# Optimization experiments

Hardware: AMD Instinct MI355X
Metric: run time of the kernel (lower is better)

Reference implementation:

```python
import jax, jax.numpy as jnp
import numpy as np

N = 32768          # nodes
LEVELS = 4         # num_sign_hops + 1
NUM_FEATURES = 512
HIDDEN = 512
VQ_DIM = 64
CODEBOOK_SIZE = 4096
VQ_WEIGHT = 0.25   # commitment_weight


def setup_inputs() -> dict:
    key = jax.random.key(0)
    ks = jax.random.split(key, 11)
    s = 0.02
    return {
        "x": jax.random.normal(ks[0], (N, LEVELS, NUM_FEATURES), jnp.float32),
        # per-level encoder: Linear(F,512) -> ReLU -> Linear(512,D)
        "enc_w1": jax.random.normal(ks[1], (LEVELS, NUM_FEATURES, HIDDEN), jnp.float32) * s,
        "enc_b1": jnp.zeros((LEVELS, HIDDEN), jnp.float32),
        "enc_w2": jax.random.normal(ks[2], (LEVELS, HIDDEN, VQ_DIM), jnp.float32) * s,
        "enc_b2": jnp.zeros((LEVELS, VQ_DIM), jnp.float32),
        # per-level decoder: Linear(D,512) -> ReLU -> Linear(512,F)
        "dec_w1": jax.random.normal(ks[3], (LEVELS, VQ_DIM, HIDDEN), jnp.float32) * s,
        "dec_b1": jnp.zeros((LEVELS, HIDDEN), jnp.float32),
        "dec_w2": jax.random.normal(ks[4], (LEVELS, HIDDEN, NUM_FEATURES), jnp.float32) * s,
        "dec_b2": jnp.zeros((LEVELS, NUM_FEATURES), jnp.float32),
        # per-level EMA codebooks (constants w.r.t. gradient in the torch module)
        "codebook": jax.random.normal(ks[5], (LEVELS, CODEBOOK_SIZE, VQ_DIM), jnp.float32),
    }


def reference(x, enc_w1, enc_b1, enc_w2, enc_b2,
              dec_w1, dec_b1, dec_w2, dec_b2, codebook):
    # Faithful to Quantizer.forward (eval mode: dropout = identity; EMA codebook
    # update is a training-time side effect, not part of the returned math).
    L = x.shape[1]
    total_mse = jnp.float32(0.0)
    commit_last = jnp.float32(0.0)
    for l in range(L):  # small fixed level count, structurally distinct params
        xl = x[:, l, :]                                   # [N, F]
        h = jax.nn.relu(xl @ enc_w1[l] + enc_b1[l])       # [N, 512]
        z = h @ enc_w2[l] + enc_b2[l]                     # [N, D]
        cb = codebook[l]                                  # [K, D]
        # squared euclidean distances [N, K] (cdist^2 via expansion)
        d = ((z * z).sum(-1, keepdims=True)
             - 2.0 * (z @ cb.T)
             + (cb * cb).sum(-1)[None, :])
        idx = jnp.argmin(d, axis=-1)                      # [N]
        q = cb[idx]                                       # [N, D] codebook lookup
        # commitment loss: mse(stop_grad(quantize), z) * weight
        commit = VQ_WEIGHT * jnp.mean((jax.lax.stop_gradient(q) - z) ** 2)
        # straight-through estimator
        quant = z + jax.lax.stop_gradient(q - z)
        h2 = jax.nn.relu(quant @ dec_w1[l] + dec_b1[l])   # [N, 512]
        x_hat = h2 @ dec_w2[l] + dec_b2[l]                # [N, F]
        total_mse = total_mse + jnp.mean((x_hat - xl) ** 2)
        commit_last = commit  # original returns LAST level's commit_loss / levels
    return (total_mse / L, commit_last / L)
```

## Files before the change

### kernel.cpp

```cpp
#include <hip/hip_runtime.h>

#define NS 32768
#define NLEV 4
#define NF 512
#define HID 512
#define VQD 64
#define CBS 4096

typedef __attribute__((ext_vector_type(8))) short bf16x8;
typedef __attribute__((ext_vector_type(4))) float f32x4;

#define MFMA16(a, b, c) __builtin_amdgcn_mfma_f32_16x16x32_bf16(a, b, c, 0, 0, 0)

__device__ inline unsigned short f2bf(float f) {
    unsigned int u = __float_as_uint(f);
    unsigned int r = (u + 0x7FFFu + ((u >> 16) & 1u)) >> 16;
    return (unsigned short)r;
}
__device__ inline float bf2f(unsigned short s) {
    return __uint_as_float(((unsigned int)s) << 16);
}

__device__ __forceinline__ void gl16(const void* g, void* l) {
    __builtin_amdgcn_global_load_lds(
        (const __attribute__((address_space(1))) unsigned int*)g,
        (__attribute__((address_space(3))) unsigned int*)l, 16, 0, 0);
}


__global__ void transpose_all(const float* __restrict__ ew1, const float* __restrict__ ew2,
                              const float* __restrict__ dw1, const float* __restrict__ dw2,
                              unsigned short* __restrict__ ew1t, unsigned short* __restrict__ ew2t,
                              unsigned short* __restrict__ dw1t, unsigned short* __restrict__ dw2t) {
    long i = (long)blockIdx.x * 256 + threadIdx.x;
    const long s1 = (long)NLEV * NF * HID;
    const long s2 = (long)NLEV * HID * VQD;
    const long s3 = (long)NLEV * VQD * HID;
    const long s4 = (long)NLEV * HID * NF;
    const float* src;
    unsigned short* dst;
    int R, C;
    if (i < s1) { src = ew1; dst = ew1t; R = NF; C = HID; }
    else if (i < s1 + s2) { i -= s1; src = ew2; dst = ew2t; R = HID; C = VQD; }
    else if (i < s1 + s2 + s3) { i -= s1 + s2; src = dw1; dst = dw1t; R = VQD; C = HID; }
    else if (i < s1 + s2 + s3 + s4) { i -= s1 + s2 + s3; src = dw2; dst = dw2t; R = HID; C = NF; }
    else return;
    int r = (int)(i % R);
    long t = i / R;
    int c = (int)(t % C);
    int b = (int)(t / C);
    dst[i] = f2bf(src[((long)b * R + r) * C + c]);
}

__global__ void cb_prep(const float* __restrict__ cb, unsigned short* __restrict__ cbb,
                        float* __restrict__ cbn) {
    int i = blockIdx.x * 256 + threadIdx.x;
    if (i >= NLEV * CBS) return;
    const float* row = cb + (long)i * VQD;
    float s = 0.f;
    for (int k = 0; k < VQD; k++) {
        float v = row[k];
        s += v * v;
        cbb[(long)i * VQD + k] = f2bf(v);
    }
    cbn[i] = s;
}

__global__ void xconv(const float* __restrict__ x, unsigned short* __restrict__ xb) {
    long i = (long)blockIdx.x * 256 + threadIdx.x;
    int l = (int)(i / ((long)NS * (NF / 8)));
    long rem = i % ((long)NS * (NF / 8));
    int n = (int)(rem >> 6);
    int f8 = ((int)rem & 63) * 8;
    const float* src = x + ((long)n * NLEV + l) * NF + f8;
    float4 f0 = *(const float4*)src;
    float4 f1 = *(const float4*)(src + 4);
    short t[8];
    t[0] = (short)f2bf(f0.x); t[1] = (short)f2bf(f0.y); t[2] = (short)f2bf(f0.z); t[3] = (short)f2bf(f0.w);
    t[4] = (short)f2bf(f1.x); t[5] = (short)f2bf(f1.y); t[6] = (short)f2bf(f1.z); t[7] = (short)f2bf(f1.w);
    *(int4*)(xb + ((long)l * NS + n) * NF + f8) = *(const int4*)t;
}

__global__ __launch_bounds__(512) void enc_fused(
    const unsigned short* __restrict__ xb, const unsigned short* __restrict__ w1t,
    const float* __restrict__ b1, const unsigned short* __restrict__ w2t,
    const float* __restrict__ b2, const unsigned short* __restrict__ cbb,
    const float* __restrict__ cbn, int* __restrict__ idxo, float* __restrict__ accum) {
    __shared__ __align__(16) short Hs[16 * 4096];
    __shared__ __align__(16) short Zst[2 * 2048];
    __shared__ float znp[2][128];
    __shared__ float zn2[128];
    __shared__ float cred;

    const int lvl = blockIdx.y;
    const int m0 = blockIdx.x * 128;
    xb += (long)lvl * NS * NF;
    w1t += (long)lvl * HID * NF;
    b1 += (long)lvl * HID;
    w2t += (long)lvl * VQD * HID;
    b2 += (long)lvl * VQD;
    cbb += (long)lvl * CBS * VQD;
    cbn += (long)lvl * CBS;
    idxo += (long)lvl * NS;

    const int tid = threadIdx.x;
    const int wave = tid >> 6, lane = tid & 63, quad = lane >> 4, lr = lane & 15;
    const int wm = wave >> 2, wn = wave & 3;
    const int lrow = lane >> 2;
    const int lcol = (lane & 3) * 8;

    if (tid == 0) cred = 0.f;

    f32x4 acc[4][4][2];
#pragma unroll
    for (int j = 0; j < 4; j++)
#pragma unroll
        for (int mt = 0; mt < 4; mt++) {
            acc[j][mt][0] = (f32x4){0.f, 0.f, 0.f, 0.f};
            acc[j][mt][1] = (f32x4){0.f, 0.f, 0.f, 0.f};
        }

    const unsigned short* ga = xb + (long)(m0 + wave * 16 + lrow) * NF + lcol;
    auto stage1 = [&](int s) {
        const int pi = s & 1;
        gl16(ga + s * 32, &Hs[pi * 4096 + wave * 16 * 32]);
#pragma unroll
        for (int j = 0; j < 4; j++)
            gl16(w1t + (long)(j * 128 + wave * 16 + lrow) * NF + s * 32 + lcol,
                 &Hs[(2 + 2 * j + pi) * 4096 + wave * 16 * 32]);
    };
    stage1(0);
#pragma unroll 2
    for (int s = 0; s < 16; s++) {
        __syncthreads();
        if (s < 15) stage1(s + 1);
        const int pi = s & 1;
        bf16x8 af[4];
#pragma unroll
        for (int mt = 0; mt < 4; mt++)
            af[mt] = *(const bf16x8*)&Hs[pi * 4096 + (wm * 64 + mt * 16 + lr) * 32 + quad * 8];
#pragma unroll
        for (int j = 0; j < 4; j++) {
            bf16x8 bf0 = *(const bf16x8*)&Hs[(2 + 2 * j + pi) * 4096 + (wn * 32 + lr) * 32 + quad * 8];
            bf16x8 bf1 = *(const bf16x8*)&Hs[(2 + 2 * j + pi) * 4096 + (wn * 32 + 16 + lr) * 32 + quad * 8];
#pragma unroll
            for (int mt = 0; mt < 4; mt++) {
                acc[j][mt][0] = MFMA16(af[mt], bf0, acc[j][mt][0]);
                acc[j][mt][1] = MFMA16(af[mt], bf1, acc[j][mt][1]);
            }
        }
    }
    __syncthreads();
#pragma unroll
    for (int j = 0; j < 4; j++) {
        float bv0 = b1[j * 128 + wn * 32 + lr];
        float bv1 = b1[j * 128 + wn * 32 + 16 + lr];
        short* hs = &Hs[(4 * j + wn) * 4096];
#pragma unroll
        for (int mt = 0; mt < 4; mt++)
#pragma unroll
            for (int r = 0; r < 4; r++) {
                int row = wm * 64 + mt * 16 + quad * 4 + r;
                float v0 = acc[j][mt][0][r] + bv0; v0 = v0 > 0.f ? v0 : 0.f;
                float v1 = acc[j][mt][1][r] + bv1; v1 = v1 > 0.f ? v1 : 0.f;
                hs[row * 32 + lr] = (short)f2bf(v0);
                hs[row * 32 + 16 + lr] = (short)f2bf(v1);
            }
    }

    f32x4 az[4];
#pragma unroll
    for (int mt = 0; mt < 4; mt++) az[mt] = (f32x4){0.f, 0.f, 0.f, 0.f};
    auto stageZ = [&](int s) {
        if (wave < 4)
            gl16(w2t + (long)(wave * 16 + lrow) * HID + s * 32 + lcol,
                 &Zst[(s & 1) * 2048 + wave * 16 * 32]);
    };
    stageZ(0);
#pragma unroll 2
    for (int s = 0; s < 16; s++) {
        __syncthreads();
        if (s < 15) stageZ(s + 1);
        bf16x8 bz = *(const bf16x8*)&Zst[(s & 1) * 2048 + (wn * 16 + lr) * 32 + quad * 8];
#pragma unroll
        for (int mt = 0; mt < 4; mt++) {
            bf16x8 af = *(const bf16x8*)&Hs[s * 4096 + (wm * 64 + mt * 16 + lr) * 32 + quad * 8];
            az[mt] = MFMA16(af, bz, az[mt]);
        }
    }
    __syncthreads();
    {
        float bz0 = b2[wn * 16 + lr];
        const int col = wn * 16 + lr;
        short* zs = &Hs[(col >> 5) * 4096];
        const int c32 = col & 31;
#pragma unroll
        for (int mt = 0; mt < 4; mt++)
#pragma unroll
            for (int r = 0; r < 4; r++) {
                int row = wm * 64 + mt * 16 + quad * 4 + r;
                zs[row * 32 + c32] = (short)f2bf(az[mt][r] + bz0);
            }
    }
    __syncthreads();

    auto stageC = [&](int t) {
        gl16(cbb + (long)(t * 64 + wn * 16 + lrow) * VQD + wm * 32 + lcol,
             &Hs[(2 + (t & 1)) * 4096 + wm * 2048 + wn * 512]);
    };
    stageC(0);
    if (tid < 256) {
        int row = tid >> 1, p = tid & 1;
        const short* zr = &Hs[p * 4096 + row * 32];
        float s2 = 0.f;
#pragma unroll
        for (int j2 = 0; j2 < 32; j2++) {
            float f = bf2f((unsigned short)zr[j2]);
            s2 += f * f;
        }
        znp[p][row] = s2;
    }
    bf16x8 a0 = *(const bf16x8*)&Hs[(wave * 16 + lr) * 32 + quad * 8];
    bf16x8 a1 = *(const bf16x8*)&Hs[4096 + (wave * 16 + lr) * 32 + quad * 8];
    __syncthreads();
    if (tid < 128) zn2[tid] = znp[0][tid] + znp[1][tid];

    float minv[4] = {1e30f, 1e30f, 1e30f, 1e30f};
    int mini[4] = {0, 0, 0, 0};
#pragma unroll 2
    for (int t = 0; t < CBS / 64; t++) {
        if (t) __syncthreads();
        if (t < CBS / 64 - 1) stageC(t + 1);
        const short* Cb = &Hs[(2 + (t & 1)) * 4096];
#pragma unroll
        for (int nt = 0; nt < 4; nt++) {
            bf16x8 c0 = *(const bf16x8*)&Cb[(nt * 16 + lr) * 32 + quad * 8];
            bf16x8 c1 = *(const bf16x8*)&Cb[2048 + (nt * 16 + lr) * 32 + quad * 8];
            f32x4 d4 = {0.f, 0.f, 0.f, 0.f};
            d4 = MFMA16(a0, c0, d4);
            d4 = MFMA16(a1, c1, d4);
            int n = t * 64 + nt * 16 + lr;
            float cn = cbn[n];
#pragma unroll
            for (int r = 0; r < 4; r++) {
                float d = fmaf(-2.f, d4[r], cn);
                if (d < minv[r]) { minv[r] = d; mini[r] = n; }
            }
        }
    }

    float csum = 0.f;
#pragma unroll
    for (int r = 0; r < 4; r++) {
        float v = minv[r];
        int ix = mini[r];
#pragma unroll
        for (int off = 8; off; off >>= 1) {
            float ov = __shfl_xor(v, off, 64);
            int oi = __shfl_xor(ix, off, 64);
            if (ov < v || (ov == v && oi < ix)) { v = ov; ix = oi; }
        }
        if (lr == 0) {
            int row = wave * 16 + quad * 4 + r;
            idxo[m0 + row] = ix;
            csum += v + zn2[row];
        }
    }
    if (lvl == NLEV - 1) {
        if (lr == 0) atomicAdd(&cred, csum);
        __syncthreads();
        if (tid == 0) atomicAdd(accum + 1, cred);
    }
}

__global__ __launch_bounds__(512) void dec_fused(
    const unsigned short* __restrict__ cbb, const int* __restrict__ idx,
    const unsigned short* __restrict__ w1t, const float* __restrict__ b1,
    const unsigned short* __restrict__ w2t, const float* __restrict__ b2,
    const unsigned short* __restrict__ xref, float* __restrict__ accum) {
    __shared__ __align__(16) short Hs[16 * 4096];
    __shared__ __align__(16) short Bst[2 * 4096];
    __shared__ float red[8];

    const int lvl = blockIdx.y;
    const int m0 = blockIdx.x * 128;
    cbb += (long)lvl * CBS * VQD;
    idx += (long)lvl * NS;
    w1t += (long)lvl * HID * VQD;
    b1 += (long)lvl * HID;
    w2t += (long)lvl * NF * HID;
    b2 += (long)lvl * NF;
    xref += (long)lvl * NS * NF;

    const int tid = threadIdx.x;
    const int wave = tid >> 6, lane = tid & 63, quad = lane >> 4, lr = lane & 15;
    const int wm = wave >> 2, wn = wave & 3;
    const int lrow = lane >> 2;
    const int lcol = (lane & 3) * 8;

    const long idxv = idx[m0 + wave * 16 + lrow];

    auto stageD = [&](int j) {
#pragma unroll
        for (int p = 0; p < 2; p++) {
            gl16(cbb + idxv * VQD + p * 32 + lcol, &Hs[(4 * j + p) * 4096 + wave * 16 * 32]);
            gl16(w1t + (long)(j * 128 + wave * 16 + lrow) * VQD + p * 32 + lcol,
                 &Hs[(4 * j + 2 + p) * 4096 + wave * 16 * 32]);
        }
    };
    stageD(0);
#pragma unroll
    for (int j = 0; j < 4; j++) {
        f32x4 acc[4][2];
#pragma unroll
        for (int mt = 0; mt < 4; mt++) {
            acc[mt][0] = (f32x4){0.f, 0.f, 0.f, 0.f};
            acc[mt][1] = (f32x4){0.f, 0.f, 0.f, 0.f};
        }
        __syncthreads();
        if (j < 3) stageD(j + 1);
#pragma unroll
        for (int p = 0; p < 2; p++) {
            bf16x8 bf0 = *(const bf16x8*)&Hs[(4 * j + 2 + p) * 4096 + (wn * 32 + lr) * 32 + quad * 8];
            bf16x8 bf1 = *(const bf16x8*)&Hs[(4 * j + 2 + p) * 4096 + (wn * 32 + 16 + lr) * 32 + quad * 8];
#pragma unroll
            for (int mt = 0; mt < 4; mt++) {
                bf16x8 af = *(const bf16x8*)&Hs[(4 * j + p) * 4096 + (wm * 64 + mt * 16 + lr) * 32 + quad * 8];
                acc[mt][0] = MFMA16(af, bf0, acc[mt][0]);
                acc[mt][1] = MFMA16(af, bf1, acc[mt][1]);
            }
        }
        __syncthreads();
        float bv0 = b1[j * 128 + wn * 32 + lr];
        float bv1 = b1[j * 128 + wn * 32 + 16 + lr];
        short* hs = &Hs[(4 * j + wn) * 4096];
#pragma unroll
        for (int mt = 0; mt < 4; mt++)
#pragma unroll
            for (int r = 0; r < 4; r++) {
                int row = wm * 64 + mt * 16 + quad * 4 + r;
                float v0 = acc[mt][0][r] + bv0; v0 = v0 > 0.f ? v0 : 0.f;
                float v1 = acc[mt][1][r] + bv1; v1 = v1 > 0.f ? v1 : 0.f;
                hs[row * 32 + lr] = (short)f2bf(v0);
                hs[row * 32 + 16 + lr] = (short)f2bf(v1);
            }
    }

    auto stageB = [&](int g) {
        gl16(w2t + (long)((g >> 4) * 128 + wave * 16 + lrow) * HID + (g & 15) * 32 + lcol,
             &Bst[(g & 1) * 4096 + wave * 16 * 32]);
    };
    stageB(0);
    float lsum = 0.f;
    f32x4 acc2[4][2];
#pragma unroll
    for (int mt = 0; mt < 4; mt++) {
        acc2[mt][0] = (f32x4){0.f, 0.f, 0.f, 0.f};
        acc2[mt][1] = (f32x4){0.f, 0.f, 0.f, 0.f};
    }
#pragma unroll 2
    for (int g = 0; g < 64; g++) {
        __syncthreads();
        if (g < 63) stageB(g + 1);
        const int s = g & 15;
        bf16x8 bf0 = *(const bf16x8*)&Bst[(g & 1) * 4096 + (wn * 32 + lr) * 32 + quad * 8];
        bf16x8 bf1 = *(const bf16x8*)&Bst[(g & 1) * 4096 + (wn * 32 + 16 + lr) * 32 + quad * 8];
#pragma unroll
        for (int mt = 0; mt < 4; mt++) {
            bf16x8 af = *(const bf16x8*)&Hs[s * 4096 + (wm * 64 + mt * 16 + lr) * 32 + quad * 8];
            acc2[mt][0] = MFMA16(af, bf0, acc2[mt][0]);
            acc2[mt][1] = MFMA16(af, bf1, acc2[mt][1]);
        }
        if (s == 15) {
            const int jj = g >> 4;
            float bv0 = b2[jj * 128 + wn * 32 + lr];
            float bv1 = b2[jj * 128 + wn * 32 + 16 + lr];
#pragma unroll
            for (int mt = 0; mt < 4; mt++)
#pragma unroll
                for (int r = 0; r < 4; r++) {
                    long row = m0 + wm * 64 + mt * 16 + quad * 4 + r;
                    int c0 = jj * 128 + wn * 32 + lr;
                    float v0 = acc2[mt][0][r] + bv0 - bf2f(xref[row * NF + c0]);
                    float v1 = acc2[mt][1][r] + bv1 - bf2f(xref[row * NF + c0 + 16]);
                    lsum += v0 * v0 + v1 * v1;
                    acc2[mt][0][r] = 0.f;
                    acc2[mt][1][r] = 0.f;
                }
        }
    }
#pragma unroll
    for (int off = 32; off; off >>= 1) lsum += __shfl_down(lsum, off, 64);
    if (lane == 0) red[wave] = lsum;
    __syncthreads();
    if (tid == 0) {
        float s2 = 0.f;
#pragma unroll
        for (int w = 0; w < 8; w++) s2 += red[w];
        atomicAdd(accum, s2);
    }
}

__global__ void finalize_k(const float* __restrict__ accum, float* __restrict__ out) {
    out[0] = accum[0] / ((float)NS * NF * NLEV);
    out[1] = 0.25f * accum[1] / ((float)NS * VQD * NLEV);
}

extern "C" void kernel_launch(void* const* d_in, const int* in_sizes, int n_in, void* d_out,
                              int out_size, void* d_ws, size_t ws_size, hipStream_t stream) {
    const float* x = (const float*)d_in[0];
    const float* enc_w1 = (const float*)d_in[1];
    const float* enc_b1 = (const float*)d_in[2];
    const float* enc_w2 = (const float*)d_in[3];
    const float* enc_b2 = (const float*)d_in[4];
    const float* dec_w1 = (const float*)d_in[5];
    const float* dec_b1 = (const float*)d_in[6];
    const float* dec_w2 = (const float*)d_in[7];
    const float* dec_b2 = (const float*)d_in[8];
    const float* cb = (const float*)d_in[9];

    char* ws = (char*)d_ws;
    size_t o = 0;
    float* accum = (float*)(ws + o); o += 256;
    unsigned short* enc_w1t = (unsigned short*)(ws + o); o += (size_t)NLEV * HID * NF * 2;
    unsigned short* enc_w2t = (unsigned short*)(ws + o); o += (size_t)NLEV * VQD * HID * 2;
    unsigned short* dec_w1t = (unsigned short*)(ws + o); o += (size_t)NLEV * HID * VQD * 2;
    unsigned short* dec_w2t = (unsigned short*)(ws + o); o += (size_t)NLEV * NF * HID * 2;
    unsigned short* cbb = (unsigned short*)(ws + o); o += (size_t)NLEV * CBS * VQD * 2;
    float* cbn = (float*)(ws + o); o += (size_t)NLEV * CBS * 4;
    unsigned short* xb = (unsigned short*)(ws + o); o += (size_t)NLEV * NS * NF * 2;
    int* idxp = (int*)(ws + o); o += (size_t)NLEV * NS * 4;

    hipMemsetAsync(accum, 0, 8, stream);

    transpose_all<<<(2 * NLEV * NF * HID + 2 * NLEV * HID * VQD + 255) / 256, 256, 0, stream>>>(
        enc_w1, enc_w2, dec_w1, dec_w2, enc_w1t, enc_w2t, dec_w1t, dec_w2t);
    cb_prep<<<(NLEV * CBS + 255) / 256, 256, 0, stream>>>(cb, cbb, cbn);
    xconv<<<(int)(((long)NLEV * NS * (NF / 8) + 255) / 256), 256, 0, stream>>>(x, xb);

    enc_fused<<<dim3(NS / 128, NLEV), 512, 0, stream>>>(
        xb, enc_w1t, enc_b1, enc_w2t, enc_b2, cbb, cbn, idxp, accum);
    dec_fused<<<dim3(NS / 128, NLEV), 512, 0, stream>>>(
        cbb, idxp, dec_w1t, dec_b1, dec_w2t, dec_b2, xb, accum);

    finalize_k<<<1, 1, 0, stream>>>(accum, (float*)d_out);
}
```

Baseline: 989.1 us.

## Replace LDS staging with direct global MFMA operand loads and shrink shared memory

The encoder and decoder kernels stop staging weights, inputs and codebook tiles through LDS with global_load_lds double buffering. MFMA operands for the first GEMM, the codebook distance search and the decoder weights are now loaded straight from global memory. Only the hidden activations stay in LDS, in an XOR-swizzled 128x128 tile, and the decoder keeps the full 128x512 output accumulator in registers. The smaller LDS footprint plus launch_bounds(512,2) aims for two blocks per CU and fewer barriers, at the cost of uncoalesced, cache-dependent global loads and high register pressure.

New measurement: 1.409 ms. 42.5% more time.

```diff
diff --git a/kernel.cpp b/kernel.cpp
--- a/kernel.cpp
+++ b/kernel.cpp
@@ -21,10 +21,13 @@
     return __uint_as_float(((unsigned int)s) << 16);
 }
 
-__device__ __forceinline__ void gl16(const void* g, void* l) {
-    __builtin_amdgcn_global_load_lds(
-        (const __attribute__((address_space(1))) unsigned int*)g,
-        (__attribute__((address_space(3))) unsigned int*)l, 16, 0, 0);
+__device__ __forceinline__ void hp_wr(short* Hp, int row, int col, float v) {
+    int byte = (row * 256 + col * 2) ^ ((row & 7) << 4);
+    *(short*)((char*)Hp + byte) = (short)f2bf(v);
+}
+__device__ __forceinline__ bf16x8 hp_rd(const short* Hp, int row, int kbyte) {
+    int byte = (row * 256 + kbyte) ^ ((row & 7) << 4);
+    return *(const bf16x8*)((const char*)Hp + byte);
 }
 
 
@@ -81,13 +84,13 @@
     *(int4*)(xb + ((long)l * NS + n) * NF + f8) = *(const int4*)t;
 }
 
-__global__ __launch_bounds__(512) void enc_fused(
+__global__ __launch_bounds__(512, 2) void enc_fused(
     const unsigned short* __restrict__ xb, const unsigned short* __restrict__ w1t,
     const float* __restrict__ b1, const unsigned short* __restrict__ w2t,
     const float* __restrict__ b2, const unsigned short* __restrict__ cbb,
     const float* __restrict__ cbn, int* __restrict__ idxo, float* __restrict__ accum) {
-    __shared__ __align__(16) short Hs[16 * 4096];
-    __shared__ __align__(16) short Zst[2 * 2048];
+    __shared__ __align__(16) short Hp[128 * 128];
+    __shared__ __align__(16) short Zs[2 * 128 * 32];
     __shared__ float znp[2][128];
     __shared__ float zn2[128];
     __shared__ float cred;
@@ -106,8 +109,6 @@
     const int tid = threadIdx.x;
     const int wave = tid >> 6, lane = tid & 63, quad = lane >> 4, lr = lane & 15;
     const int wm = wave >> 2, wn = wave & 3;
-    const int lrow = lane >> 2;
-    const int lcol = (lane & 3) * 8;
 
     if (tid == 0) cred = 0.f;
 
@@ -120,29 +121,18 @@
             acc[j][mt][1] = (f32x4){0.f, 0.f, 0.f, 0.f};
         }
 
-    const unsigned short* ga = xb + (long)(m0 + wave * 16 + lrow) * NF + lcol;
-    auto stage1 = [&](int s) {
-        const int pi = s & 1;
-        gl16(ga + s * 32, &Hs[pi * 4096 + wave * 16 * 32]);
-#pragma unroll
-        for (int j = 0; j < 4; j++)
-            gl16(w1t + (long)(j * 128 + wave * 16 + lrow) * NF + s * 32 + lcol,
-                 &Hs[(2 + 2 * j + pi) * 4096 + wave * 16 * 32]);
-    };
-    stage1(0);
+    const unsigned short* pa = xb + (long)(m0 + wm * 64 + lr) * NF + quad * 8;
+    const unsigned short* pb = w1t + (long)(wn * 32 + lr) * NF + quad * 8;
 #pragma unroll 2
     for (int s = 0; s < 16; s++) {
-        __syncthreads();
-        if (s < 15) stage1(s + 1);
-        const int pi = s & 1;
         bf16x8 af[4];
 #pragma unroll
         for (int mt = 0; mt < 4; mt++)
-            af[mt] = *(const bf16x8*)&Hs[pi * 4096 + (wm * 64 + mt * 16 + lr) * 32 + quad * 8];
+            af[mt] = *(const bf16x8*)(pa + (long)mt * 16 * NF + s * 32);
 #pragma unroll
         for (int j = 0; j < 4; j++) {
-            bf16x8 bf0 = *(const bf16x8*)&Hs[(2 + 2 * j + pi) * 4096 + (wn * 32 + lr) * 32 + quad * 8];
-            bf16x8 bf1 = *(const bf16x8*)&Hs[(2 + 2 * j + pi) * 4096 + (wn * 32 + 16 + lr) * 32 + quad * 8];
+            bf16x8 bf0 = *(const bf16x8*)(pb + (long)j * 128 * NF + s * 32);
+            bf16x8 bf1 = *(const bf16x8*)(pb + (long)(j * 128 + 16) * NF + s * 32);
 #pragma unroll
             for (int mt = 0; mt < 4; mt++) {
                 acc[j][mt][0] = MFMA16(af[mt], bf0, acc[j][mt][0]);
@@ -150,12 +140,16 @@
             }
         }
     }
-    __syncthreads();
+
+    f32x4 az[4];
+#pragma unroll
+    for (int mt = 0; mt < 4; mt++) az[mt] = (f32x4){0.f, 0.f, 0.f, 0.f};
+
 #pragma unroll
     for (int j = 0; j < 4; j++) {
+        if (j) __syncthreads();
         float bv0 = b1[j * 128 + wn * 32 + lr];
         float bv1 = b1[j * 128 + wn * 32 + 16 + lr];
-        short* hs = &Hs[(4 * j + wn) * 4096];
 #pragma unroll
         for (int mt = 0; mt < 4; mt++)
 #pragma unroll
@@ -163,36 +157,25 @@
                 int row = wm * 64 + mt * 16 + quad * 4 + r;
                 float v0 = acc[j][mt][0][r] + bv0; v0 = v0 > 0.f ? v0 : 0.f;
                 float v1 = acc[j][mt][1][r] + bv1; v1 = v1 > 0.f ? v1 : 0.f;
-                hs[row * 32 + lr] = (short)f2bf(v0);
-                hs[row * 32 + 16 + lr] = (short)f2bf(v1);
-            }
-    }
-
-    f32x4 az[4];
-#pragma unroll
-    for (int mt = 0; mt < 4; mt++) az[mt] = (f32x4){0.f, 0.f, 0.f, 0.f};
-    auto stageZ = [&](int s) {
-        if (wave < 4)
-            gl16(w2t + (long)(wave * 16 + lrow) * HID + s * 32 + lcol,
-                 &Zst[(s & 1) * 2048 + wave * 16 * 32]);
-    };
-    stageZ(0);
-#pragma unroll 2
-    for (int s = 0; s < 16; s++) {
+                hp_wr(Hp, row, wn * 32 + lr, v0);
+                hp_wr(Hp, row, wn * 32 + 16 + lr, v1);
+            }
         __syncthreads();
-        if (s < 15) stageZ(s + 1);
-        bf16x8 bz = *(const bf16x8*)&Zst[(s & 1) * 2048 + (wn * 16 + lr) * 32 + quad * 8];
-#pragma unroll
-        for (int mt = 0; mt < 4; mt++) {
-            bf16x8 af = *(const bf16x8*)&Hs[s * 4096 + (wm * 64 + mt * 16 + lr) * 32 + quad * 8];
-            az[mt] = MFMA16(af, bz, az[mt]);
-        }
-    }
-    __syncthreads();
+#pragma unroll
+        for (int s = 0; s < 4; s++) {
+            bf16x8 bz = *(const bf16x8*)&w2t[(long)(wn * 16 + lr) * HID + j * 128 + s * 32 + quad * 8];
+#pragma unroll
+            for (int mt = 0; mt < 4; mt++) {
+                bf16x8 afz = hp_rd(Hp, wm * 64 + mt * 16 + lr, s * 64 + quad * 16);
+                az[mt] = MFMA16(afz, bz, az[mt]);
+            }
+        }
+    }
+
     {
         float bz0 = b2[wn * 16 + lr];
         const int col = wn * 16 + lr;
-        short* zs = &Hs[(col >> 5) * 4096];
+        short* zs = &Zs[(col >> 5) * 4096];
         const int c32 = col & 31;
 #pragma unroll
         for (int mt = 0; mt < 4; mt++)
@@ -204,14 +187,9 @@
     }
     __syncthreads();
 
-    auto stageC = [&](int t) {
-        gl16(cbb + (long)(t * 64 + wn * 16 + lrow) * VQD + wm * 32 + lcol,
-             &Hs[(2 + (t & 1)) * 4096 + wm * 2048 + wn * 512]);
-    };
-    stageC(0);
     if (tid < 256) {
         int row = tid >> 1, p = tid & 1;
-        const short* zr = &Hs[p * 4096 + row * 32];
+        const short* zr = &Zs[p * 4096 + row * 32];
         float s2 = 0.f;
 #pragma unroll
         for (int j2 = 0; j2 < 32; j2++) {
@@ -220,8 +198,8 @@
         }
         znp[p][row] = s2;
     }
-    bf16x8 a0 = *(const bf16x8*)&Hs[(wave * 16 + lr) * 32 + quad * 8];
-    bf16x8 a1 = *(const bf16x8*)&Hs[4096 + (wave * 16 + lr) * 32 + quad * 8];
+    bf16x8 a0 = *(const bf16x8*)&Zs[(wave * 16 + lr) * 32 + quad * 8];
+    bf16x8 a1 = *(const bf16x8*)&Zs[4096 + (wave * 16 + lr) * 32 + quad * 8];
     __syncthreads();
     if (tid < 128) zn2[tid] = znp[0][tid] + znp[1][tid];
 
@@ -229,18 +207,16 @@
     int mini[4] = {0, 0, 0, 0};
 #pragma unroll 2
     for (int t = 0; t < CBS / 64; t++) {
-        if (t) __syncthreads();
-        if (t < CBS / 64 - 1) stageC(t + 1);
-        const short* Cb = &Hs[(2 + (t & 1)) * 4096];
 #pragma unroll
         for (int nt = 0; nt < 4; nt++) {
-            bf16x8 c0 = *(const bf16x8*)&Cb[(nt * 16 + lr) * 32 + quad * 8];
-            bf16x8 c1 = *(const bf16x8*)&Cb[2048 + (nt * 16 + lr) * 32 + quad * 8];
+            const unsigned short* cr = cbb + (long)(t * 64 + nt * 16 + lr) * VQD + quad * 8;
+            bf16x8 c0 = *(const bf16x8*)cr;
+            bf16x8 c1 = *(const bf16x8*)(cr + 32);
+            int n = t * 64 + nt * 16 + lr;
+            float cn = cbn[n];
             f32x4 d4 = {0.f, 0.f, 0.f, 0.f};
             d4 = MFMA16(a0, c0, d4);
             d4 = MFMA16(a1, c1, d4);
-            int n = t * 64 + nt * 16 + lr;
-            float cn = cbn[n];
 #pragma unroll
             for (int r = 0; r < 4; r++) {
                 float d = fmaf(-2.f, d4[r], cn);
@@ -273,13 +249,12 @@
     }
 }
 
-__global__ __launch_bounds__(512) void dec_fused(
+__global__ __launch_bounds__(512, 2) void dec_fused(
     const unsigned short* __restrict__ cbb, const int* __restrict__ idx,
     const unsigned short* __restrict__ w1t, const float* __restrict__ b1,
     const unsigned short* __restrict__ w2t, const float* __restrict__ b2,
     const unsigned short* __restrict__ xref, float* __restrict__ accum) {
-    __shared__ __align__(16) short Hs[16 * 4096];
-    __shared__ __align__(16) short Bst[2 * 4096];
+    __shared__ __align__(16) short Hp[128 * 128];
     __shared__ float red[8];
 
     const int lvl = blockIdx.y;
@@ -295,99 +270,81 @@
     const int tid = threadIdx.x;
     const int wave = tid >> 6, lane = tid & 63, quad = lane >> 4, lr = lane & 15;
     const int wm = wave >> 2, wn = wave & 3;
-    const int lrow = lane >> 2;
-    const int lcol = (lane & 3) * 8;
-
-    const long idxv = idx[m0 + wave * 16 + lrow];
-
-    auto stageD = [&](int j) {
+
+    int iv[4];
+#pragma unroll
+    for (int mt = 0; mt < 4; mt++) iv[mt] = idx[m0 + wm * 64 + mt * 16 + lr];
+
+    f32x4 acc2[4][8];
+#pragma unroll
+    for (int mt = 0; mt < 4; mt++)
+#pragma unroll
+        for (int nt = 0; nt < 8; nt++) acc2[mt][nt] = (f32x4){0.f, 0.f, 0.f, 0.f};
+
+#pragma unroll
+    for (int j = 0; j < 4; j++) {
+        f32x4 ap[4][2];
+#pragma unroll
+        for (int mt = 0; mt < 4; mt++) {
+            ap[mt][0] = (f32x4){0.f, 0.f, 0.f, 0.f};
+            ap[mt][1] = (f32x4){0.f, 0.f, 0.f, 0.f};
+        }
 #pragma unroll
         for (int p = 0; p < 2; p++) {
-            gl16(cbb + idxv * VQD + p * 32 + lcol, &Hs[(4 * j + p) * 4096 + wave * 16 * 32]);
-            gl16(w1t + (long)(j * 128 + wave * 16 + lrow) * VQD + p * 32 + lcol,
-                 &Hs[(4 * j + 2 + p) * 4096 + wave * 16 * 32]);
-        }
-    };
-    stageD(0);
-#pragma unroll
-    for (int j = 0; j < 4; j++) {
-        f32x4 acc[4][2];
-#pragma unroll
-        for (int mt = 0; mt < 4; mt++) {
-            acc[mt][0] = (f32x4){0.f, 0.f, 0.f, 0.f};
-            acc[mt][1] = (f32x4){0.f, 0.f, 0.f, 0.f};
-        }
-        __syncthreads();
-        if (j < 3) stageD(j + 1);
-#pragma unroll
-        for (int p = 0; p < 2; p++) {
-            bf16x8 bf0 = *(const bf16x8*)&Hs[(4 * j + 2 + p) * 4096 + (wn * 32 + lr) * 32 + quad * 8];
-            bf16x8 bf1 = *(const bf16x8*)&Hs[(4 * j + 2 + p) * 4096 + (wn * 32 + 16 + lr) * 32 + quad * 8];
+            bf16x8 bfn[2];
+#pragma unroll
+            for (int nt = 0; nt < 2; nt++)
+                bfn[nt] = *(const bf16x8*)&w1t[(long)(j * 128 + wn * 32 + nt * 16 + lr) * VQD + p * 32 + quad * 8];
 #pragma unroll
             for (int mt = 0; mt < 4; mt++) {
-                bf16x8 af = *(const bf16x8*)&Hs[(4 * j + p) * 4096 + (wm * 64 + mt * 16 + lr) * 32 + quad * 8];
-                acc[mt][0] = MFMA16(af, bf0, acc[mt][0]);
-                acc[mt][1] = MFMA16(af, bf1, acc[mt][1]);
-            }
-        }
-        __syncthreads();
+                bf16x8 af = *(const bf16x8*)&cbb[(long)iv[mt] * VQD + p * 32 + quad * 8];
+                ap[mt][0] = MFMA16(af, bfn[0], ap[mt][0]);
+                ap[mt][1] = MFMA16(af, bfn[1], ap[mt][1]);
+            }
+        }
+        if (j) __syncthreads();
         float bv0 = b1[j * 128 + wn * 32 + lr];
         float bv1 = b1[j * 128 + wn * 32 + 16 + lr];
-        short* hs = &Hs[(4 * j + wn) * 4096];
 #pragma unroll
         for (int mt = 0; mt < 4; mt++)
 #pragma unroll
             for (int r = 0; r < 4; r++) {
                 int row = wm * 64 + mt * 16 + quad * 4 + r;
-                float v0 = acc[mt][0][r] + bv0; v0 = v0 > 0.f ? v0 : 0.f;
-                float v1 = acc[mt][1][r] + bv1; v1 = v1 > 0.f ? v1 : 0.f;
-                hs[row * 32 + lr] = (short)f2bf(v0);
-                hs[row * 32 + 16 + lr] = (short)f2bf(v1);
-            }
-    }
-
-    auto stageB = [&](int g) {
-        gl16(w2t + (long)((g >> 4) * 128 + wave * 16 + lrow) * HID + (g & 15) * 32 + lcol,
-             &Bst[(g & 1) * 4096 + wave * 16 * 32]);
-    };
-    stageB(0);
+                float v0 = ap[mt][0][r] + bv0; v0 = v0 > 0.f ? v0 : 0.f;
+                float v1 = ap[mt][1][r] + bv1; v1 = v1 > 0.f ? v1 : 0.f;
+                hp_wr(Hp, row, wn * 32 + lr, v0);
+                hp_wr(Hp, row, wn * 32 + 16 + lr, v1);
+            }
+        __syncthreads();
+#pragma unroll
+        for (int s = 0; s < 4; s++) {
+            bf16x8 af2[4];
+#pragma unroll
+            for (int mt = 0; mt < 4; mt++)
+                af2[mt] = hp_rd(Hp, wm * 64 + mt * 16 + lr, s * 64 + quad * 16);
+#pragma unroll
+            for (int nt = 0; nt < 8; nt++) {
+                bf16x8 bfr = *(const bf16x8*)&w2t[(long)(wn * 128 + nt * 16 + lr) * HID + j * 128 + s * 32 + quad * 8];
+#pragma unroll
+                for (int mt = 0; mt < 4; mt++)
+                    acc2[mt][nt] = MFMA16(af2[mt], bfr, acc2[mt][nt]);
+            }
+        }
+    }
+
     float lsum = 0.f;
-    f32x4 acc2[4][2];
-#pragma unroll
-    for (int mt = 0; mt < 4; mt++) {
-        acc2[mt][0] = (f32x4){0.f, 0.f, 0.f, 0.f};
-        acc2[mt][1] = (f32x4){0.f, 0.f, 0.f, 0.f};
-    }
-#pragma unroll 2
-    for (int g = 0; g < 64; g++) {
-        __syncthreads();
-        if (g < 63) stageB(g + 1);
-        const int s = g & 15;
-        bf16x8 bf0 = *(const bf16x8*)&Bst[(g & 1) * 4096 + (wn * 32 + lr) * 32 + quad * 8];
-        bf16x8 bf1 = *(const bf16x8*)&Bst[(g & 1) * 4096 + (wn * 32 + 16 + lr) * 32 + quad * 8];
-#pragma unroll
-        for (int mt = 0; mt < 4; mt++) {
-            bf16x8 af = *(const bf16x8*)&Hs[s * 4096 + (wm * 64 + mt * 16 + lr) * 32 + quad * 8];
-            acc2[mt][0] = MFMA16(af, bf0, acc2[mt][0]);
-            acc2[mt][1] = MFMA16(af, bf1, acc2[mt][1]);
-        }
-        if (s == 15) {
-            const int jj = g >> 4;
-            float bv0 = b2[jj * 128 + wn * 32 + lr];
-            float bv1 = b2[jj * 128 + wn * 32 + 16 + lr];
-#pragma unroll
-            for (int mt = 0; mt < 4; mt++)
-#pragma unroll
-                for (int r = 0; r < 4; r++) {
-                    long row = m0 + wm * 64 + mt * 16 + quad * 4 + r;
-                    int c0 = jj * 128 + wn * 32 + lr;
-                    float v0 = acc2[mt][0][r] + bv0 - bf2f(xref[row * NF + c0]);
-                    float v1 = acc2[mt][1][r] + bv1 - bf2f(xref[row * NF + c0 + 16]);
-                    lsum += v0 * v0 + v1 * v1;
-                    acc2[mt][0][r] = 0.f;
-                    acc2[mt][1][r] = 0.f;
-                }
-        }
+#pragma unroll
+    for (int nt = 0; nt < 8; nt++) {
+        int col = wn * 128 + nt * 16 + lr;
+        float bv = b2[col];
+#pragma unroll
+        for (int mt = 0; mt < 4; mt++)
+#pragma unroll
+            for (int r = 0; r < 4; r++) {
+                long row = m0 + wm * 64 + mt * 16 + quad * 4 + r;
+                float v = acc2[mt][nt][r] + bv - bf2f(xref[row * NF + col]);
+                lsum += v * v;
+            }
     }
 #pragma unroll
     for (int off = 32; off; off >>= 1) lsum += __shfl_down(lsum, off, 64);
```
